# Kernel tuning notes

Hardware: AMD Instinct MI355X
Metric: run time of the kernel (lower is better)

Reference implementation:

```python
import jax, jax.numpy as jnp
import numpy as np

MAX_DIST = 35.0
GRID_RES = 1.0
BOX = int(np.ceil(2 * MAX_DIST / GRID_RES + 1))  # 71


def setup_inputs() -> dict:
    key = jax.random.key(0)
    k1, k2 = jax.random.split(key)
    B, N, F = 8, 16384, 32
    # spread ~N(0, 20): most points inside [-35, 35] box, some outside (mask path)
    coords = jax.random.normal(k1, (B, N, 3), dtype=jnp.float32) * 20.0
    features = jax.random.normal(k2, (B, N, F), dtype=jnp.float32)
    return {"coords": coords, "features": features}


def reference(coords, features):
    B, N, _ = coords.shape
    F = features.shape[2]
    # quantize coords to integer grid cells
    gc = jnp.round((coords + MAX_DIST) / GRID_RES).astype(jnp.int32)  # [B,N,3]
    in_box = jnp.all((gc >= 0) & (gc < BOX), axis=2)                  # [B,N]
    # jit-friendly equivalent of boolean_mask+scatter_nd: zero out-of-box
    # updates and clamp their indices (adding zero is a no-op).
    gc_c = jnp.clip(gc, 0, BOX - 1)
    upd = jnp.where(in_box[..., None], features, 0.0)                 # [B,N,F]
    grid = jnp.zeros((B, BOX, BOX, BOX, F), dtype=features.dtype)
    # FAITHFUL to original: batch index column is tf.zeros -> every point
    # scatters (with duplicate-index summation) into batch slice 0.
    grid = grid.at[0, gc_c[..., 0], gc_c[..., 1], gc_c[..., 2]].add(upd)
    return grid
```

## Files before the change

### kernel.cpp

```cpp
#include <hip/hip_runtime.h>

#define BOX 71
#define NF 32
#define MAX_DIST_F 35.0f
#define SLICE_FLOATS (BOX * BOX * BOX * NF)

typedef float vfloat4 __attribute__((ext_vector_type(4)));

__global__ __launch_bounds__(256) void MakeGrid_zero_slice0(
    vfloat4* __restrict__ out, int n4)
{
    int stride = gridDim.x * blockDim.x;
    vfloat4 z = {0.f, 0.f, 0.f, 0.f};
    for (int i = blockIdx.x * blockDim.x + threadIdx.x; i < n4; i += stride)
        out[i] = z;
}

__global__ __launch_bounds__(256) void MakeGrid_fused_scatter_zero(
    const float* __restrict__ coords,
    const float* __restrict__ features,
    float* __restrict__ grid,
    vfloat4* __restrict__ rest,
    size_t rest_n4,
    int total_tasks)
{
    int b = blockIdx.x;
    int tid = threadIdx.x;

    if ((b & 3) == 0) {
        int sb = b >> 2;
        int stride = (gridDim.x >> 2) * blockDim.x;
        for (int t = sb * blockDim.x + tid; t < total_tasks; t += stride) {
            int p = t >> 5;
            int f = t & 31;

            float cx = coords[p * 3 + 0];
            float cy = coords[p * 3 + 1];
            float cz = coords[p * 3 + 2];

            int gx = (int)rintf(cx + MAX_DIST_F);
            int gy = (int)rintf(cy + MAX_DIST_F);
            int gz = (int)rintf(cz + MAX_DIST_F);

            bool in_box = (gx >= 0) & (gx < BOX) &
                          (gy >= 0) & (gy < BOX) &
                          (gz >= 0) & (gz < BOX);
            if (!in_box) continue;

            float v = features[(size_t)p * NF + f];
            size_t idx = (((size_t)gx * BOX + gy) * BOX + gz) * NF + f;
            atomicAdd(grid + idx, v);
        }
    } else {
        size_t zb = (size_t)(b >> 2) * 3 + (size_t)(b & 3) - 1;
        size_t nzb = ((size_t)gridDim.x >> 2) * 3;
        size_t stride = nzb * blockDim.x;
        vfloat4 z = {0.f, 0.f, 0.f, 0.f};
        for (size_t i = zb * blockDim.x + tid; i < rest_n4; i += stride)
            __builtin_nontemporal_store(z, &rest[i]);
    }
}

extern "C" void kernel_launch(void* const* d_in, const int* in_sizes, int n_in,
                              void* d_out, int out_size, void* d_ws, size_t ws_size,
                              hipStream_t stream) {
    const float* coords   = (const float*)d_in[0];
    const float* features = (const float*)d_in[1];
    float* out = (float*)d_out;

    int total_points = in_sizes[0] / 3;
    int total_tasks = total_points * NF;

    int slice0_n4 = SLICE_FLOATS / 4;
    MakeGrid_zero_slice0<<<4096, 256, 0, stream>>>((vfloat4*)out, slice0_n4);

    size_t rest_n4 = ((size_t)out_size - SLICE_FLOATS) / 4;
    vfloat4* rest = (vfloat4*)(out + SLICE_FLOATS);

    MakeGrid_fused_scatter_zero<<<8192, 256, 0, stream>>>(
        coords, features, out, rest, rest_n4, total_tasks);
}
```

Measured before the change: 388.1 us.

## Bin points per cell then gather-accumulate instead of per-feature atomics

Adds a binning pass that records point indices per grid cell in fixed-capacity buckets, with an overflow list handled by a small atomic kernel. The accumulation kernel then sums features per cell and writes slice 0 directly, replacing millions of float atomics and the separate slice-0 zeroing pass. It costs extra workspace, a count-zeroing kernel and more launches, and relies on the workspace being large enough, with a fallback otherwise.

```diff
diff --git a/kernel.cpp b/kernel.cpp
--- a/kernel.cpp
+++ b/kernel.cpp
@@ -2,63 +2,127 @@
 
 #define BOX 71
 #define NF 32
+#define CELLS (BOX * BOX * BOX)
+#define SLICE_FLOATS (CELLS * NF)
 #define MAX_DIST_F 35.0f
-#define SLICE_FLOATS (BOX * BOX * BOX * NF)
+#define CAP 8
+#define OVF_MAX 65536
 
 typedef float vfloat4 __attribute__((ext_vector_type(4)));
+typedef int   vint4   __attribute__((ext_vector_type(4)));
 
-__global__ __launch_bounds__(256) void MakeGrid_zero_slice0(
-    vfloat4* __restrict__ out, int n4)
+#define COUNTS_PAD_INTS 357912
+#define OFF_BUCKETS (COUNTS_PAD_INTS * 4)
+#define OFF_OVFCNT  (OFF_BUCKETS + CELLS * CAP * 4)
+#define OFF_OVFLIST (OFF_OVFCNT + 16)
+#define WS_NEEDED   (OFF_OVFLIST + OVF_MAX * 4)
+
+__device__ __forceinline__ int cell_of(const float* coords, int p, bool* in_box) {
+    int gx = (int)rintf(coords[p * 3 + 0] + MAX_DIST_F);
+    int gy = (int)rintf(coords[p * 3 + 1] + MAX_DIST_F);
+    int gz = (int)rintf(coords[p * 3 + 2] + MAX_DIST_F);
+    *in_box = (gx >= 0) & (gx < BOX) & (gy >= 0) & (gy < BOX) & (gz >= 0) & (gz < BOX);
+    return (gx * BOX + gy) * BOX + gz;
+}
+
+__global__ __launch_bounds__(256) void MakeGrid_zero_ws(
+    vint4* __restrict__ counts4, int n4, int* __restrict__ ovfcnt)
 {
     int stride = gridDim.x * blockDim.x;
-    vfloat4 z = {0.f, 0.f, 0.f, 0.f};
+    vint4 z = {0, 0, 0, 0};
     for (int i = blockIdx.x * blockDim.x + threadIdx.x; i < n4; i += stride)
-        out[i] = z;
+        counts4[i] = z;
+    if (blockIdx.x == 0 && threadIdx.x == 0) *ovfcnt = 0;
 }
 
-__global__ __launch_bounds__(256) void MakeGrid_fused_scatter_zero(
-    const float* __restrict__ coords,
+__global__ __launch_bounds__(256) void MakeGrid_bin(
+    const float* __restrict__ coords, int total_points,
+    int* __restrict__ counts, int* __restrict__ buckets,
+    int* __restrict__ ovfcnt, int* __restrict__ ovflist)
+{
+    int p = blockIdx.x * blockDim.x + threadIdx.x;
+    if (p >= total_points) return;
+    bool in_box;
+    int cell = cell_of(coords, p, &in_box);
+    if (!in_box) return;
+    int r = atomicAdd(&counts[cell], 1);
+    if (r < CAP) {
+        buckets[cell * CAP + r] = p;
+    } else {
+        int o = atomicAdd(ovfcnt, 1);
+        if (o < OVF_MAX) ovflist[o] = p;
+    }
+}
+
+__global__ __launch_bounds__(256) void MakeGrid_accum_zero(
     const float* __restrict__ features,
+    const int* __restrict__ counts, const int* __restrict__ buckets,
     float* __restrict__ grid,
     vfloat4* __restrict__ rest,
-    size_t rest_n4,
-    int total_tasks)
+    size_t rest_n4)
 {
-    int b = blockIdx.x;
-    int tid = threadIdx.x;
-
+    int b = blockIdx.x, tid = threadIdx.x;
     if ((b & 3) == 0) {
         int sb = b >> 2;
-        int stride = (gridDim.x >> 2) * blockDim.x;
-        for (int t = sb * blockDim.x + tid; t < total_tasks; t += stride) {
-            int p = t >> 5;
-            int f = t & 31;
-
-            float cx = coords[p * 3 + 0];
-            float cy = coords[p * 3 + 1];
-            float cz = coords[p * 3 + 2];
-
-            int gx = (int)rintf(cx + MAX_DIST_F);
-            int gy = (int)rintf(cy + MAX_DIST_F);
-            int gz = (int)rintf(cz + MAX_DIST_F);
-
-            bool in_box = (gx >= 0) & (gx < BOX) &
-                          (gy >= 0) & (gy < BOX) &
-                          (gz >= 0) & (gz < BOX);
-            if (!in_box) continue;
-
-            float v = features[(size_t)p * NF + f];
-            size_t idx = (((size_t)gx * BOX + gy) * BOX + gz) * NF + f;
-            atomicAdd(grid + idx, v);
+        int group = tid >> 5, f = tid & 31;
+        int cstride = (gridDim.x >> 2) * 8;
+        for (int cell = sb * 8 + group; cell < CELLS; cell += cstride) {
+            int c = counts[cell];
+            c = c > CAP ? CAP : c;
+            float s = 0.f;
+            const int* bk = &buckets[(size_t)cell * CAP];
+            for (int i = 0; i < c; ++i) {
+                int p = bk[i];
+                s += features[(size_t)p * NF + f];
+            }
+            __builtin_nontemporal_store(s, &grid[(size_t)cell * NF + f]);
         }
     } else {
         size_t zb = (size_t)(b >> 2) * 3 + (size_t)(b & 3) - 1;
-        size_t nzb = ((size_t)gridDim.x >> 2) * 3;
-        size_t stride = nzb * blockDim.x;
+        size_t stride = ((size_t)gridDim.x >> 2) * 3 * blockDim.x;
         vfloat4 z = {0.f, 0.f, 0.f, 0.f};
         for (size_t i = zb * blockDim.x + tid; i < rest_n4; i += stride)
             __builtin_nontemporal_store(z, &rest[i]);
     }
+}
+
+__global__ __launch_bounds__(256) void MakeGrid_overflow(
+    const float* __restrict__ coords, const float* __restrict__ features,
+    float* __restrict__ grid,
+    const int* __restrict__ ovfcnt, const int* __restrict__ ovflist)
+{
+    int n = *ovfcnt;
+    n = n > OVF_MAX ? OVF_MAX : n;
+    int total = n * NF;
+    int stride = gridDim.x * blockDim.x;
+    for (int t = blockIdx.x * blockDim.x + threadIdx.x; t < total; t += stride) {
+        int p = ovflist[t >> 5], f = t & 31;
+        bool in_box;
+        int cell = cell_of(coords, p, &in_box);
+        atomicAdd(&grid[(size_t)cell * NF + f], features[(size_t)p * NF + f]);
+    }
+}
+
+__global__ __launch_bounds__(256) void MakeGrid_zero_all(
+    vfloat4* __restrict__ out, size_t n4)
+{
+    size_t stride = (size_t)gridDim.x * blockDim.x;
+    vfloat4 z = {0.f, 0.f, 0.f, 0.f};
+    for (size_t i = (size_t)blockIdx.x * blockDim.x + threadIdx.x; i < n4; i += stride)
+        out[i] = z;
+}
+
+__global__ __launch_bounds__(256) void MakeGrid_scatter_atomic(
+    const float* __restrict__ coords, const float* __restrict__ features,
+    float* __restrict__ grid, int total_points)
+{
+    int t = blockIdx.x * blockDim.x + threadIdx.x;
+    int p = t >> 5, f = t & 31;
+    if (p >= total_points) return;
+    bool in_box;
+    int cell = cell_of(coords, p, &in_box);
+    if (!in_box) return;
+    atomicAdd(&grid[(size_t)cell * NF + f], features[(size_t)p * NF + f]);
 }
 
 extern "C" void kernel_launch(void* const* d_in, const int* in_sizes, int n_in,
@@ -69,14 +133,31 @@
     float* out = (float*)d_out;
 
     int total_points = in_sizes[0] / 3;
-    int total_tasks = total_points * NF;
 
-    int slice0_n4 = SLICE_FLOATS / 4;
-    MakeGrid_zero_slice0<<<4096, 256, 0, stream>>>((vfloat4*)out, slice0_n4);
+    if (ws_size >= (size_t)WS_NEEDED) {
+        char* ws = (char*)d_ws;
+        int* counts  = (int*)ws;
+        int* buckets = (int*)(ws + OFF_BUCKETS);
+        int* ovfcnt  = (int*)(ws + OFF_OVFCNT);
+        int* ovflist = (int*)(ws + OFF_OVFLIST);
 
-    size_t rest_n4 = ((size_t)out_size - SLICE_FLOATS) / 4;
-    vfloat4* rest = (vfloat4*)(out + SLICE_FLOATS);
+        MakeGrid_zero_ws<<<128, 256, 0, stream>>>(
+            (vint4*)counts, COUNTS_PAD_INTS / 4, ovfcnt);
 
-    MakeGrid_fused_scatter_zero<<<8192, 256, 0, stream>>>(
-        coords, features, out, rest, rest_n4, total_tasks);
+        MakeGrid_bin<<<(total_points + 255) / 256, 256, 0, stream>>>(
+            coords, total_points, counts, buckets, ovfcnt, ovflist);
+
+        size_t rest_n4 = ((size_t)out_size - SLICE_FLOATS) / 4;
+        MakeGrid_accum_zero<<<8192, 256, 0, stream>>>(
+            features, counts, buckets, out,
+            (vfloat4*)(out + SLICE_FLOATS), rest_n4);
+
+        MakeGrid_overflow<<<64, 256, 0, stream>>>(
+            coords, features, out, ovfcnt, ovflist);
+    } else {
+        MakeGrid_zero_all<<<8192, 256, 0, stream>>>((vfloat4*)out, (size_t)out_size / 4);
+        int total_threads = total_points * NF;
+        MakeGrid_scatter_atomic<<<(total_threads + 255) / 256, 256, 0, stream>>>(
+            coords, features, out, total_points);
+    }
 }
```

Measured after the change: 468.2 us. 1.21x slower.
